# Performance work log

Hardware: AMD Instinct MI355X
Metric: run time of the kernel (lower is better)

## Reference

```python
import jax, jax.numpy as jnp
import numpy as np
import math

PHI = (1.0 + math.sqrt(5.0)) / 2.0
LUT_N = 4096
_TWO_PI = 2.0 * math.pi
_ang = np.arange(LUT_N, dtype=np.float32) * (_TWO_PI / LUT_N)
SIN_T = jnp.asarray(np.sin(_ang), dtype=jnp.float32)
COS_T = jnp.asarray(np.cos(_ang), dtype=jnp.float32)


def lookup_sin_cos(theta):
    # Linearly-interpolated 4096-entry sin/cos LUT over [0, 2pi)
    pos = theta * (LUT_N / _TWO_PI)
    i0f = jnp.floor(pos)
    frac = pos - i0f
    i0 = i0f.astype(jnp.int32) % LUT_N
    i1 = (i0 + 1) % LUT_N
    sin = SIN_T[i0] * (1.0 - frac) + SIN_T[i1] * frac
    cos = COS_T[i0] * (1.0 - frac) + COS_T[i1] * frac
    return sin, cos


def setup_inputs() -> dict:
    key = jax.random.key(0)
    ks = jax.random.split(key, 10)
    B, D, H = 8192, 1024, 4
    dh = D // H
    return {
        "x_real": jax.random.normal(ks[0], (B, D), dtype=jnp.float32),
        "x_imag": jax.random.normal(ks[1], (B, D), dtype=jnp.float32),
        "t": jax.random.uniform(ks[2], (B,), dtype=jnp.float32) * 100.0,
        "trigger_real": jax.random.normal(ks[3], (H, dh), dtype=jnp.float32) * 0.5,
        "trigger_imag": jax.random.normal(ks[4], (H, dh), dtype=jnp.float32) * 0.5,
        "w_query": jax.random.normal(ks[5], (H, dh), dtype=jnp.float32) * 0.02,
        "b_query": jnp.zeros((H, dh), dtype=jnp.float32),
        "w_out": jax.random.normal(ks[6], (D,), dtype=jnp.float32) * 0.02,
        "b_out": jnp.zeros((D,), dtype=jnp.float32),
        "beta": jnp.abs(jax.random.normal(ks[7], (D,), dtype=jnp.float32)) * 5.0 + 5.0,
    }


def reference(x_real, x_imag, t, trigger_real, trigger_imag, w_query, b_query,
              w_out, b_out, beta):
    B, D = x_real.shape
    H, dh = trigger_real.shape
    t_phi = (t * PHI)[:, None]            # (B, 1)

    # ---- per-head conjugate interference ----
    xr = x_real.reshape(B, H, dh)
    xi = x_imag.reshape(B, H, dh)
    wl_q = 1.0 + jnp.abs(w_query)          # (H, dh)
    tp = t_phi[:, :, None]                 # (B, 1, 1)
    th_r = xr / wl_q + b_query + tp        # (B, H, dh)
    th_i = xi / wl_q + b_query + tp
    sin_r, cos_r = lookup_sin_cos(th_r)
    sin_i, cos_i = lookup_sin_cos(th_i)
    q_r = cos_r * cos_i - sin_r * sin_i
    q_i = cos_r * sin_i + sin_r * cos_i
    int_r = (q_r * trigger_real + q_i * trigger_imag).sum(-1)   # (B, H)
    int_i = (q_r * trigger_imag - q_i * trigger_real).sum(-1)   # (B, H)
    tot_r = int_r.mean(-1)                 # (B,)
    tot_i = int_i.mean(-1)
    mag = jnp.sqrt(tot_r * tot_r + tot_i * tot_i + 1e-8)[:, None]  # (B, 1)

    # ---- gated Q-EMA memory update (memory starts at zeros) ----
    beta_eff = 1.0 / (1.0 + jnp.abs(beta))     # (D,)
    w_eff = 1.0 / (1.0 + jnp.abs(w_out))       # (D,)
    decay = jnp.minimum(jnp.exp(-beta_eff * w_eff), 0.9999)
    write_scale = w_eff * (1.0 - decay)        # (D,)
    # initial memory is zero, so memory*decay term vanishes
    mem_r = x_real * mag * write_scale
    mem_i = x_imag * mag * write_scale

    # ---- Euler output projection ----
    wl_out = 1.0 + jnp.abs(w_out)
    to_r = mem_r / wl_out + b_out + t_phi
    to_i = mem_i / wl_out + b_out + t_phi
    s_or, c_or = lookup_sin_cos(to_r)
    s_oi, c_oi = lookup_sin_cos(to_i)
    out_real = c_or * c_oi - s_or * s_oi
    out_imag = c_or * s_oi + s_or * c_oi
    return out_real, out_imag
```

## Files before the change

kernel.cpp:

```cpp
#include <hip/hip_runtime.h>
#include <math.h>

#define DCOLS 1024
#define PHI_F 1.61803398874989484820f

__global__ __launch_bounds__(256, 2) void echo_kernel(
    const float* __restrict__ x_real, const float* __restrict__ x_imag,
    const float* __restrict__ t,
    const float* __restrict__ trig_r, const float* __restrict__ trig_i,
    const float* __restrict__ w_query, const float* __restrict__ b_query,
    const float* __restrict__ w_out, const float* __restrict__ b_out,
    const float* __restrict__ beta,
    float* __restrict__ out_real, float* __restrict__ out_imag,
    int B, int total_waves)
{
    const int tid  = threadIdx.x;
    const int lane = tid & 63;
    const int wid  = tid >> 6;
    const int wave = (blockIdx.x << 2) + wid;
    const int c0   = lane << 2;

    float invq[16], addq[16], trr[16], tri[16], c2[16], addo[16];
    #pragma unroll
    for (int k = 0; k < 4; ++k) {
        const int c = (k << 8) + c0;
        const float4 wq = *reinterpret_cast<const float4*>(w_query + c);
        const float4 bq = *reinterpret_cast<const float4*>(b_query + c);
        const float4 tr = *reinterpret_cast<const float4*>(trig_r  + c);
        const float4 ti = *reinterpret_cast<const float4*>(trig_i  + c);
        const float4 wo = *reinterpret_cast<const float4*>(w_out   + c);
        const float4 bo = *reinterpret_cast<const float4*>(b_out   + c);
        const float4 be = *reinterpret_cast<const float4*>(beta    + c);
        #pragma unroll
        for (int j = 0; j < 4; ++j) {
            const int e = (k << 2) + j;
            invq[e] = __builtin_amdgcn_rcpf(1.0f + fabsf((&wq.x)[j]));
            addq[e] = 2.0f * (&bq.x)[j];
            trr[e]  = (&tr.x)[j];
            tri[e]  = (&ti.x)[j];
            const float weff  = __builtin_amdgcn_rcpf(1.0f + fabsf((&wo.x)[j]));
            const float beff  = __builtin_amdgcn_rcpf(1.0f + fabsf((&be.x)[j]));
            const float decay = fminf(__expf(-beff * weff), 0.9999f);
            c2[e]   = weff * weff * (1.0f - decay);
            addo[e] = 2.0f * (&bo.x)[j];
        }
    }

    int row = wave;
    if (row >= B) return;
    long base = (long)row * DCOLS + c0;

    float4 xr[4], xi[4];
    #pragma unroll
    for (int k = 0; k < 4; ++k) {
        xr[k] = *reinterpret_cast<const float4*>(x_real + base + (k << 8));
        xi[k] = *reinterpret_cast<const float4*>(x_imag + base + (k << 8));
    }
    float tcur = t[row];

    while (true) {
        const int  nrow = row + total_waves;
        const bool more = (nrow < B);
        const float tphi2 = 2.0f * PHI_F * tcur;

        float s[16];
        float tot_r = 0.f, tot_i = 0.f;
        #pragma unroll
        for (int k = 0; k < 4; ++k) {
            #pragma unroll
            for (int j = 0; j < 4; ++j) {
                const int e = (k << 2) + j;
                const float sv = (&xr[k].x)[j] + (&xi[k].x)[j];
                s[e] = sv;
                const float ang = fmaf(sv, invq[e], addq[e] + tphi2);
                float sn, cs;
                __sincosf(ang, &sn, &cs);
                tot_r = fmaf(cs, trr[e], fmaf(sn, tri[e], tot_r));
                tot_i = fmaf(cs, tri[e], fmaf(-sn, trr[e], tot_i));
            }
        }

        float4 nxr[4], nxi[4];
        float tnext = 0.f;
        const long nbase = (long)nrow * DCOLS + c0;
        if (more) {
            #pragma unroll
            for (int k = 0; k < 4; ++k) {
                nxr[k] = *reinterpret_cast<const float4*>(x_real + nbase + (k << 8));
                nxi[k] = *reinterpret_cast<const float4*>(x_imag + nbase + (k << 8));
            }
            tnext = t[nrow];
        }

        #pragma unroll
        for (int m = 32; m >= 1; m >>= 1) {
            tot_r += __shfl_xor(tot_r, m, 64);
            tot_i += __shfl_xor(tot_i, m, 64);
        }
        const float TR = tot_r * 0.25f, TI = tot_i * 0.25f;
        const float mag = sqrtf(fmaf(TR, TR, fmaf(TI, TI, 1e-8f)));

        #pragma unroll
        for (int k = 0; k < 4; ++k) {
            float4 o_r, o_i;
            #pragma unroll
            for (int j = 0; j < 4; ++j) {
                const int e = (k << 2) + j;
                const float ang = fmaf(s[e], mag * c2[e], addo[e] + tphi2);
                float sn, cs;
                __sincosf(ang, &sn, &cs);
                (&o_r.x)[j] = cs;
                (&o_i.x)[j] = sn;
            }
            *reinterpret_cast<float4*>(out_real + base + (k << 8)) = o_r;
            *reinterpret_cast<float4*>(out_imag + base + (k << 8)) = o_i;
        }

        if (!more) break;
        row = nrow; base = nbase; tcur = tnext;
        #pragma unroll
        for (int k = 0; k < 4; ++k) { xr[k] = nxr[k]; xi[k] = nxi[k]; }
    }
}

extern "C" void kernel_launch(void* const* d_in, const int* in_sizes, int n_in,
                              void* d_out, int out_size, void* d_ws, size_t ws_size,
                              hipStream_t stream) {
    const float* x_real = (const float*)d_in[0];
    const float* x_imag = (const float*)d_in[1];
    const float* t      = (const float*)d_in[2];
    const float* trig_r = (const float*)d_in[3];
    const float* trig_i = (const float*)d_in[4];
    const float* w_q    = (const float*)d_in[5];
    const float* b_q    = (const float*)d_in[6];
    const float* w_out  = (const float*)d_in[7];
    const float* b_out  = (const float*)d_in[8];
    const float* beta   = (const float*)d_in[9];

    const int B = in_sizes[2];
    float* out_real = (float*)d_out;
    float* out_imag = (float*)d_out + (long)B * DCOLS;

    const int blocks = (B + 15) / 16;
    const int total_waves = blocks * 4;

    echo_kernel<<<blocks, 256, 0, stream>>>(x_real, x_imag, t,
                                            trig_r, trig_i, w_q, b_q,
                                            w_out, b_out, beta,
                                            out_real, out_imag,
                                            B, total_waves);
}
```

Before: 129.9 us.

## Use one row per wave with recomputed constants and nontemporal loads/stores

Drops the persistent grid-stride loop with software prefetch and launches one wave per row, so the grid grows from B/16 to B/4 blocks. The per-column constants are now reloaded and recomputed per row instead of held in registers, and launch bounds are raised to 4 blocks per SM to get more occupancy. Input loads and output stores use nontemporal hints to avoid polluting the cache with streamed data. The trade is extra redundant constant loads and transcendental work per row, in exchange for lower register pressure and more waves in flight to hide memory latency.

```diff
diff --git a/kernel.cpp b/kernel.cpp
--- a/kernel.cpp
+++ b/kernel.cpp
@@ -4,7 +4,9 @@
 #define DCOLS 1024
 #define PHI_F 1.61803398874989484820f
 
-__global__ __launch_bounds__(256, 2) void echo_kernel(
+typedef float vf4 __attribute__((ext_vector_type(4)));
+
+__global__ __launch_bounds__(256, 4) void echo_kernel(
     const float* __restrict__ x_real, const float* __restrict__ x_imag,
     const float* __restrict__ t,
     const float* __restrict__ trig_r, const float* __restrict__ trig_i,
@@ -12,114 +14,78 @@
     const float* __restrict__ w_out, const float* __restrict__ b_out,
     const float* __restrict__ beta,
     float* __restrict__ out_real, float* __restrict__ out_imag,
-    int B, int total_waves)
+    int B)
 {
     const int tid  = threadIdx.x;
     const int lane = tid & 63;
     const int wid  = tid >> 6;
-    const int wave = (blockIdx.x << 2) + wid;
-    const int c0   = lane << 2;
+    const int row  = (blockIdx.x << 2) + wid;
+    if (row >= B) return;
+    const int  c0   = lane << 2;
+    const long base = (long)row * DCOLS + c0;
 
-    float invq[16], addq[16], trr[16], tri[16], c2[16], addo[16];
+    vf4 xr[4], xi[4];
+    #pragma unroll
+    for (int k = 0; k < 4; ++k) {
+        xr[k] = __builtin_nontemporal_load(
+                    reinterpret_cast<const vf4*>(x_real + base + (k << 8)));
+        xi[k] = __builtin_nontemporal_load(
+                    reinterpret_cast<const vf4*>(x_imag + base + (k << 8)));
+    }
+    const float tphi2 = 2.0f * PHI_F * t[row];
+
+    float tot_r = 0.f, tot_i = 0.f;
     #pragma unroll
     for (int k = 0; k < 4; ++k) {
         const int c = (k << 8) + c0;
-        const float4 wq = *reinterpret_cast<const float4*>(w_query + c);
-        const float4 bq = *reinterpret_cast<const float4*>(b_query + c);
-        const float4 tr = *reinterpret_cast<const float4*>(trig_r  + c);
-        const float4 ti = *reinterpret_cast<const float4*>(trig_i  + c);
-        const float4 wo = *reinterpret_cast<const float4*>(w_out   + c);
-        const float4 bo = *reinterpret_cast<const float4*>(b_out   + c);
-        const float4 be = *reinterpret_cast<const float4*>(beta    + c);
+        const vf4 wq = *reinterpret_cast<const vf4*>(w_query + c);
+        const vf4 bq = *reinterpret_cast<const vf4*>(b_query + c);
+        const vf4 tr = *reinterpret_cast<const vf4*>(trig_r  + c);
+        const vf4 ti = *reinterpret_cast<const vf4*>(trig_i  + c);
         #pragma unroll
         for (int j = 0; j < 4; ++j) {
-            const int e = (k << 2) + j;
-            invq[e] = __builtin_amdgcn_rcpf(1.0f + fabsf((&wq.x)[j]));
-            addq[e] = 2.0f * (&bq.x)[j];
-            trr[e]  = (&tr.x)[j];
-            tri[e]  = (&ti.x)[j];
-            const float weff  = __builtin_amdgcn_rcpf(1.0f + fabsf((&wo.x)[j]));
-            const float beff  = __builtin_amdgcn_rcpf(1.0f + fabsf((&be.x)[j]));
-            const float decay = fminf(__expf(-beff * weff), 0.9999f);
-            c2[e]   = weff * weff * (1.0f - decay);
-            addo[e] = 2.0f * (&bo.x)[j];
+            const float sv  = xr[k][j] + xi[k][j];
+            const float ang = fmaf(sv, __builtin_amdgcn_rcpf(1.0f + fabsf(wq[j])),
+                                   fmaf(2.0f, bq[j], tphi2));
+            float sn, cs;
+            __sincosf(ang, &sn, &cs);
+            tot_r = fmaf(cs, tr[j], fmaf(sn, ti[j], tot_r));
+            tot_i = fmaf(cs, ti[j], fmaf(-sn, tr[j], tot_i));
         }
     }
 
-    int row = wave;
-    if (row >= B) return;
-    long base = (long)row * DCOLS + c0;
+    #pragma unroll
+    for (int m = 32; m >= 1; m >>= 1) {
+        tot_r += __shfl_xor(tot_r, m, 64);
+        tot_i += __shfl_xor(tot_i, m, 64);
+    }
+    const float TR = tot_r * 0.25f, TI = tot_i * 0.25f;
+    const float mag = sqrtf(fmaf(TR, TR, fmaf(TI, TI, 1e-8f)));
 
-    float4 xr[4], xi[4];
     #pragma unroll
     for (int k = 0; k < 4; ++k) {
-        xr[k] = *reinterpret_cast<const float4*>(x_real + base + (k << 8));
-        xi[k] = *reinterpret_cast<const float4*>(x_imag + base + (k << 8));
-    }
-    float tcur = t[row];
-
-    while (true) {
-        const int  nrow = row + total_waves;
-        const bool more = (nrow < B);
-        const float tphi2 = 2.0f * PHI_F * tcur;
-
-        float s[16];
-        float tot_r = 0.f, tot_i = 0.f;
+        const int c = (k << 8) + c0;
+        const vf4 wo = *reinterpret_cast<const vf4*>(w_out + c);
+        const vf4 bo = *reinterpret_cast<const vf4*>(b_out + c);
+        const vf4 be = *reinterpret_cast<const vf4*>(beta  + c);
+        vf4 o_r, o_i;
         #pragma unroll
-        for (int k = 0; k < 4; ++k) {
-            #pragma unroll
-            for (int j = 0; j < 4; ++j) {
-                const int e = (k << 2) + j;
-                const float sv = (&xr[k].x)[j] + (&xi[k].x)[j];
-                s[e] = sv;
-                const float ang = fmaf(sv, invq[e], addq[e] + tphi2);
-                float sn, cs;
-                __sincosf(ang, &sn, &cs);
-                tot_r = fmaf(cs, trr[e], fmaf(sn, tri[e], tot_r));
-                tot_i = fmaf(cs, tri[e], fmaf(-sn, trr[e], tot_i));
-            }
+        for (int j = 0; j < 4; ++j) {
+            const float weff  = __builtin_amdgcn_rcpf(1.0f + fabsf(wo[j]));
+            const float beff  = __builtin_amdgcn_rcpf(1.0f + fabsf(be[j]));
+            const float decay = fminf(__expf(-beff * weff), 0.9999f);
+            const float sv    = xr[k][j] + xi[k][j];
+            const float ang   = fmaf(sv, mag * weff * weff * (1.0f - decay),
+                                     fmaf(2.0f, bo[j], tphi2));
+            float sn, cs;
+            __sincosf(ang, &sn, &cs);
+            o_r[j] = cs;
+            o_i[j] = sn;
         }
-
-        float4 nxr[4], nxi[4];
-        float tnext = 0.f;
-        const long nbase = (long)nrow * DCOLS + c0;
-        if (more) {
-            #pragma unroll
-            for (int k = 0; k < 4; ++k) {
-                nxr[k] = *reinterpret_cast<const float4*>(x_real + nbase + (k << 8));
-                nxi[k] = *reinterpret_cast<const float4*>(x_imag + nbase + (k << 8));
-            }
-            tnext = t[nrow];
-        }
-
-        #pragma unroll
-        for (int m = 32; m >= 1; m >>= 1) {
-            tot_r += __shfl_xor(tot_r, m, 64);
-            tot_i += __shfl_xor(tot_i, m, 64);
-        }
-        const float TR = tot_r * 0.25f, TI = tot_i * 0.25f;
-        const float mag = sqrtf(fmaf(TR, TR, fmaf(TI, TI, 1e-8f)));
-
-        #pragma unroll
-        for (int k = 0; k < 4; ++k) {
-            float4 o_r, o_i;
-            #pragma unroll
-            for (int j = 0; j < 4; ++j) {
-                const int e = (k << 2) + j;
-                const float ang = fmaf(s[e], mag * c2[e], addo[e] + tphi2);
-                float sn, cs;
-                __sincosf(ang, &sn, &cs);
-                (&o_r.x)[j] = cs;
-                (&o_i.x)[j] = sn;
-            }
-            *reinterpret_cast<float4*>(out_real + base + (k << 8)) = o_r;
-            *reinterpret_cast<float4*>(out_imag + base + (k << 8)) = o_i;
-        }
-
-        if (!more) break;
-        row = nrow; base = nbase; tcur = tnext;
-        #pragma unroll
-        for (int k = 0; k < 4; ++k) { xr[k] = nxr[k]; xi[k] = nxi[k]; }
+        __builtin_nontemporal_store(o_r,
+            reinterpret_cast<vf4*>(out_real + base + (k << 8)));
+        __builtin_nontemporal_store(o_i,
+            reinterpret_cast<vf4*>(out_imag + base + (k << 8)));
     }
 }
 
@@ -141,12 +107,10 @@
     float* out_real = (float*)d_out;
     float* out_imag = (float*)d_out + (long)B * DCOLS;
 
-    const int blocks = (B + 15) / 16;
-    const int total_waves = blocks * 4;
+    const int blocks = (B + 3) >> 2;
 
     echo_kernel<<<blocks, 256, 0, stream>>>(x_real, x_imag, t,
                                             trig_r, trig_i, w_q, b_q,
                                             w_out, b_out, beta,
-                                            out_real, out_imag,
-                                            B, total_waves);
+                                            out_real, out_imag, B);
 }
```

Result: slower. 142.0 us (+9.3%).

## Fold row phase into rotated triggers, reuse input registers, raise occupancy

Applied to the files above, without the earlier changes.

Since the interference magnitude is invariant to a common phase rotation, the per-row t*phi term is dropped from the first sincos and the bias term is folded into pre-rotated trigger weights. The input sums are computed before the next row's prefetch so the same registers are reused instead of separate next-row buffers. Launch bounds raise occupancy and the grid is doubled so each wave processes fewer rows. This trims per-element arithmetic and register pressure, at the cost of slight numerical differences from the reordered phase math.

```diff
diff --git a/kernel.cpp b/kernel.cpp
--- a/kernel.cpp
+++ b/kernel.cpp
@@ -4,7 +4,9 @@
 #define DCOLS 1024
 #define PHI_F 1.61803398874989484820f
 
-__global__ __launch_bounds__(256, 2) void echo_kernel(
+typedef float vf4 __attribute__((ext_vector_type(4)));
+
+__global__ __launch_bounds__(256, 3) void echo_kernel(
     const float* __restrict__ x_real, const float* __restrict__ x_imag,
     const float* __restrict__ t,
     const float* __restrict__ trig_r, const float* __restrict__ trig_i,
@@ -20,29 +22,30 @@
     const int wave = (blockIdx.x << 2) + wid;
     const int c0   = lane << 2;
 
-    float invq[16], addq[16], trr[16], tri[16], c2[16], addo[16];
+    float invq[16], trr[16], tri[16], c2[16], addo[16];
     #pragma unroll
     for (int k = 0; k < 4; ++k) {
         const int c = (k << 8) + c0;
-        const float4 wq = *reinterpret_cast<const float4*>(w_query + c);
-        const float4 bq = *reinterpret_cast<const float4*>(b_query + c);
-        const float4 tr = *reinterpret_cast<const float4*>(trig_r  + c);
-        const float4 ti = *reinterpret_cast<const float4*>(trig_i  + c);
-        const float4 wo = *reinterpret_cast<const float4*>(w_out   + c);
-        const float4 bo = *reinterpret_cast<const float4*>(b_out   + c);
-        const float4 be = *reinterpret_cast<const float4*>(beta    + c);
+        const vf4 wq = *reinterpret_cast<const vf4*>(w_query + c);
+        const vf4 bq = *reinterpret_cast<const vf4*>(b_query + c);
+        const vf4 tr = *reinterpret_cast<const vf4*>(trig_r  + c);
+        const vf4 ti = *reinterpret_cast<const vf4*>(trig_i  + c);
+        const vf4 wo = *reinterpret_cast<const vf4*>(w_out   + c);
+        const vf4 bo = *reinterpret_cast<const vf4*>(b_out   + c);
+        const vf4 be = *reinterpret_cast<const vf4*>(beta    + c);
         #pragma unroll
         for (int j = 0; j < 4; ++j) {
             const int e = (k << 2) + j;
-            invq[e] = __builtin_amdgcn_rcpf(1.0f + fabsf((&wq.x)[j]));
-            addq[e] = 2.0f * (&bq.x)[j];
-            trr[e]  = (&tr.x)[j];
-            tri[e]  = (&ti.x)[j];
-            const float weff  = __builtin_amdgcn_rcpf(1.0f + fabsf((&wo.x)[j]));
-            const float beff  = __builtin_amdgcn_rcpf(1.0f + fabsf((&be.x)[j]));
+            invq[e] = __builtin_amdgcn_rcpf(1.0f + fabsf(wq[j]));
+            float sA, cA;
+            __sincosf(2.0f * bq[j], &sA, &cA);
+            trr[e] = fmaf(tr[j], cA,  ti[j] * sA);
+            tri[e] = fmaf(ti[j], cA, -tr[j] * sA);
+            const float weff  = __builtin_amdgcn_rcpf(1.0f + fabsf(wo[j]));
+            const float beff  = __builtin_amdgcn_rcpf(1.0f + fabsf(be[j]));
             const float decay = fminf(__expf(-beff * weff), 0.9999f);
             c2[e]   = weff * weff * (1.0f - decay);
-            addo[e] = 2.0f * (&bo.x)[j];
+            addo[e] = 2.0f * bo[j];
         }
     }
 
@@ -50,46 +53,45 @@
     if (row >= B) return;
     long base = (long)row * DCOLS + c0;
 
-    float4 xr[4], xi[4];
+    vf4 xr[4], xi[4];
     #pragma unroll
     for (int k = 0; k < 4; ++k) {
-        xr[k] = *reinterpret_cast<const float4*>(x_real + base + (k << 8));
-        xi[k] = *reinterpret_cast<const float4*>(x_imag + base + (k << 8));
+        xr[k] = *reinterpret_cast<const vf4*>(x_real + base + (k << 8));
+        xi[k] = *reinterpret_cast<const vf4*>(x_imag + base + (k << 8));
     }
     float tcur = t[row];
 
     while (true) {
         const int  nrow = row + total_waves;
         const bool more = (nrow < B);
+
+        float s[16];
+        #pragma unroll
+        for (int k = 0; k < 4; ++k)
+            #pragma unroll
+            for (int j = 0; j < 4; ++j)
+                s[(k << 2) + j] = xr[k][j] + xi[k][j];
+
         const float tphi2 = 2.0f * PHI_F * tcur;
 
-        float s[16];
-        float tot_r = 0.f, tot_i = 0.f;
-        #pragma unroll
-        for (int k = 0; k < 4; ++k) {
-            #pragma unroll
-            for (int j = 0; j < 4; ++j) {
-                const int e = (k << 2) + j;
-                const float sv = (&xr[k].x)[j] + (&xi[k].x)[j];
-                s[e] = sv;
-                const float ang = fmaf(sv, invq[e], addq[e] + tphi2);
-                float sn, cs;
-                __sincosf(ang, &sn, &cs);
-                tot_r = fmaf(cs, trr[e], fmaf(sn, tri[e], tot_r));
-                tot_i = fmaf(cs, tri[e], fmaf(-sn, trr[e], tot_i));
-            }
-        }
-
-        float4 nxr[4], nxi[4];
+        const long nbase = (long)nrow * DCOLS + c0;
         float tnext = 0.f;
-        const long nbase = (long)nrow * DCOLS + c0;
         if (more) {
             #pragma unroll
             for (int k = 0; k < 4; ++k) {
-                nxr[k] = *reinterpret_cast<const float4*>(x_real + nbase + (k << 8));
-                nxi[k] = *reinterpret_cast<const float4*>(x_imag + nbase + (k << 8));
+                xr[k] = *reinterpret_cast<const vf4*>(x_real + nbase + (k << 8));
+                xi[k] = *reinterpret_cast<const vf4*>(x_imag + nbase + (k << 8));
             }
             tnext = t[nrow];
+        }
+
+        float tot_r = 0.f, tot_i = 0.f;
+        #pragma unroll
+        for (int e = 0; e < 16; ++e) {
+            float sn, cs;
+            __sincosf(s[e] * invq[e], &sn, &cs);
+            tot_r = fmaf(cs, trr[e], fmaf(sn, tri[e], tot_r));
+            tot_i = fmaf(cs, tri[e], fmaf(-sn, trr[e], tot_i));
         }
 
         #pragma unroll
@@ -102,24 +104,22 @@
 
         #pragma unroll
         for (int k = 0; k < 4; ++k) {
-            float4 o_r, o_i;
+            vf4 o_r, o_i;
             #pragma unroll
             for (int j = 0; j < 4; ++j) {
                 const int e = (k << 2) + j;
                 const float ang = fmaf(s[e], mag * c2[e], addo[e] + tphi2);
                 float sn, cs;
                 __sincosf(ang, &sn, &cs);
-                (&o_r.x)[j] = cs;
-                (&o_i.x)[j] = sn;
+                o_r[j] = cs;
+                o_i[j] = sn;
             }
-            *reinterpret_cast<float4*>(out_real + base + (k << 8)) = o_r;
-            *reinterpret_cast<float4*>(out_imag + base + (k << 8)) = o_i;
+            *reinterpret_cast<vf4*>(out_real + base + (k << 8)) = o_r;
+            *reinterpret_cast<vf4*>(out_imag + base + (k << 8)) = o_i;
         }
 
         if (!more) break;
         row = nrow; base = nbase; tcur = tnext;
-        #pragma unroll
-        for (int k = 0; k < 4; ++k) { xr[k] = nxr[k]; xi[k] = nxi[k]; }
     }
 }
 
@@ -141,7 +141,7 @@
     float* out_real = (float*)d_out;
     float* out_imag = (float*)d_out + (long)B * DCOLS;
 
-    const int blocks = (B + 15) / 16;
+    const int blocks = (B + 7) >> 3;
     const int total_waves = blocks * 4;
 
     echo_kernel<<<blocks, 256, 0, stream>>>(x_real, x_imag, t,
```

Result: slower. 134.6 us (+3.6%).
